# Kernel tuning notes

Hardware: AMD Instinct MI355X
Metric: run time of the kernel (lower is better)

The kernel has to match this reference:

```python
import jax, jax.numpy as jnp
import numpy as np

D_MODEL = 1024
N_HEADS = 2
D_FF = 4096
SEQ = 4096
HEAD_DIM = D_MODEL // N_HEADS
SCALE = HEAD_DIM ** 0.5
LN_EPS = 1e-5


def _layer_norm(x, g, b):
    mu = jnp.mean(x, axis=-1, keepdims=True)
    var = jnp.mean(jnp.square(x - mu), axis=-1, keepdims=True)
    return (x - mu) * jax.lax.rsqrt(var + LN_EPS) * g + b


def _gelu_tanh(x):
    # torch nn.GELU(approximate='tanh')
    c = np.sqrt(2.0 / np.pi).astype(np.float32)
    return 0.5 * x * (1.0 + jnp.tanh(c * (x + 0.044715 * x * x * x)))


def setup_inputs() -> dict:
    key = jax.random.key(0)
    ks = jax.random.split(key, 12)
    s = 1.0 / np.sqrt(D_MODEL)
    sf = 1.0 / np.sqrt(D_FF)
    inp = {
        "x": jax.random.normal(ks[0], (SEQ, D_MODEL), jnp.float32),
        "ln1_g": jnp.ones((D_MODEL,), jnp.float32),
        "ln1_b": jnp.zeros((D_MODEL,), jnp.float32),
        "wq": jax.random.normal(ks[1], (D_MODEL, D_MODEL), jnp.float32) * s,
        "bq": jnp.zeros((D_MODEL,), jnp.float32),
        "wk": jax.random.normal(ks[2], (D_MODEL, D_MODEL), jnp.float32) * s,
        "bk": jnp.zeros((D_MODEL,), jnp.float32),
        "wv": jax.random.normal(ks[3], (D_MODEL, D_MODEL), jnp.float32) * s,
        "bv": jnp.zeros((D_MODEL,), jnp.float32),
        "wo": jax.random.normal(ks[4], (D_MODEL, D_MODEL), jnp.float32) * s,
        "bo": jnp.zeros((D_MODEL,), jnp.float32),
        "ln2_g": jnp.ones((D_MODEL,), jnp.float32),
        "ln2_b": jnp.zeros((D_MODEL,), jnp.float32),
        "w1": jax.random.normal(ks[5], (D_FF, D_MODEL), jnp.float32) * s,
        "b1": jnp.zeros((D_FF,), jnp.float32),
        "w2": jax.random.normal(ks[6], (D_MODEL, D_FF), jnp.float32) * sf,
        "b2": jnp.zeros((D_MODEL,), jnp.float32),
    }
    return inp


def reference(x, ln1_g, ln1_b, wq, bq, wk, bk, wv, bv, wo, bo,
              ln2_g, ln2_b, w1, b1, w2, b2):
    S = x.shape[0]
    h = _layer_norm(x, ln1_g, ln1_b)
    # torch Linear: y = h @ W.T + b
    q = h @ wq.T + bq
    k = h @ wk.T + bk
    v = h @ wv.T + bv
    # chunk(2, dim=-1) == reshape last dim to (heads, head_dim)
    qh = q.reshape(S, N_HEADS, HEAD_DIM)
    kh = k.reshape(S, N_HEADS, HEAD_DIM)
    vh = v.reshape(S, N_HEADS, HEAD_DIM)
    scores = jnp.einsum('shd,thd->hst', qh, kh) / SCALE  # [H,S,S]
    attn = jax.nn.softmax(scores, axis=-1)
    o = jnp.einsum('hst,thd->shd', attn, vh).reshape(S, D_MODEL)
    x = x + (o @ wo.T + bo)
    h2 = _layer_norm(x, ln2_g, ln2_b)
    ff = _gelu_tanh(h2 @ w1.T + b1) @ w2.T + b2
    return x + ff
```

## Files before the change

### kernel.cpp

```cpp
#include <hip/hip_runtime.h>
#include <math.h>

#define SEQ 4096
#define DM  1024
#define DFF 4096
#define NH  2
#define HD  512

typedef unsigned short ushort_t;
typedef short  s16x8 __attribute__((ext_vector_type(8)));
typedef float  f32x4 __attribute__((ext_vector_type(4)));
typedef unsigned short u16x8 __attribute__((ext_vector_type(8)));

__device__ __forceinline__ float bf2f(unsigned short u) {
    return __uint_as_float(((unsigned)u) << 16);
}
__device__ __forceinline__ unsigned short f2bf(float f) {
    unsigned u = __float_as_uint(f);
    unsigned r = (u + 0x7fffu + ((u >> 16) & 1u)) >> 16;
    return (unsigned short)r;
}

__device__ __forceinline__ void async_load16(void* lds, const void* g) {
    __builtin_amdgcn_global_load_lds(
        (const __attribute__((address_space(1))) void*)g,
        (__attribute__((address_space(3))) void*)lds, 16, 0, 0);
}

template<bool HAS_BIAS, bool DO_GELU, bool HAS_RES, bool OUT_BF16, int SPLITS, int MODE>
__global__ __launch_bounds__(256)
void gemm_nt(const ushort_t* __restrict__ A, int lda,
             const ushort_t* __restrict__ B, int ldb,
             void* __restrict__ Cv, int ldc,
             const float* __restrict__ bias,
             const float* __restrict__ res, int ldres,
             int K, float alpha,
             size_t strA, size_t strB, size_t strC, size_t strBias,
             float* __restrict__ rowsum)
{
    __shared__ alignas(16) ushort_t sA[128 * 64];
    __shared__ alignas(16) ushort_t sB[128 * 64];

    const int z  = blockIdx.z;
    const int zb = z / SPLITS;
    const int ks = (z % SPLITS) * K;
    A += (size_t)zb * strA;
    B += (size_t)zb * strB;
    if (HAS_BIAS) bias += (size_t)zb * strBias;

    const int tid   = threadIdx.x;
    const int lane  = tid & 63;
    const int wave  = tid >> 6;
    const int waveM = wave >> 1, waveN = wave & 1;
    const int m0 = blockIdx.y * 128, n0 = blockIdx.x * 128;
    const int lr = lane & 15, quad = lane >> 4;

    f32x4 acc[4][4] = {};

    const ushort_t* Ag = A + (size_t)m0 * lda + ks;
    const ushort_t* Bg = B + (size_t)n0 * ldb + ks;

    const int ldRow = (lane >> 3);
    const int ldCol = (((lane & 7) ^ (lane >> 3)) * 8);

    for (int k0 = 0; k0 < K; k0 += 64) {
#pragma unroll
        for (int i = 0; i < 4; ++i) {
            int r = wave * 32 + i * 8 + ldRow;
            async_load16(&sA[(wave * 32 + i * 8) * 64],
                         Ag + (size_t)r * lda + k0 + ldCol);
            async_load16(&sB[(wave * 32 + i * 8) * 64],
                         Bg + (size_t)r * ldb + k0 + ldCol);
        }
        __syncthreads();

#pragma unroll
        for (int kk = 0; kk < 64; kk += 32) {
            const int pg = ((((kk >> 3) + quad) ^ (lr & 7)) << 3);
            s16x8 af[4], bfr[4];
#pragma unroll
            for (int mi = 0; mi < 4; ++mi)
                af[mi] = *(const s16x8*)&sA[(waveM * 64 + mi * 16 + lr) * 64 + pg];
#pragma unroll
            for (int ni = 0; ni < 4; ++ni)
                bfr[ni] = *(const s16x8*)&sB[(waveN * 64 + ni * 16 + lr) * 64 + pg];
#pragma unroll
            for (int mi = 0; mi < 4; ++mi)
#pragma unroll
                for (int ni = 0; ni < 4; ++ni)
                    acc[mi][ni] = __builtin_amdgcn_mfma_f32_16x16x32_bf16(
                        af[mi], bfr[ni], acc[mi][ni], 0, 0, 0);
        }
        __syncthreads();
    }

    float rs_part[4][4];
    if (MODE == 1) {
#pragma unroll
        for (int mi = 0; mi < 4; ++mi)
#pragma unroll
            for (int r = 0; r < 4; ++r) rs_part[mi][r] = 0.0f;
    }

#pragma unroll
    for (int mi = 0; mi < 4; ++mi) {
#pragma unroll
        for (int r = 0; r < 4; ++r) {
            int row = m0 + waveM * 64 + mi * 16 + quad * 4 + r;
#pragma unroll
            for (int ni = 0; ni < 4; ++ni) {
                int col = n0 + waveN * 64 + ni * 16 + lr;
                float v = acc[mi][ni][r] * alpha;
                if (HAS_BIAS) v += bias[col];
                if (DO_GELU) {
                    float xx = v;
                    float inner = 0.7978845608028654f * (xx + 0.044715f * xx * xx * xx);
                    v = 0.5f * xx * (1.0f + tanhf(inner));
                }
                if (HAS_RES) v += res[(size_t)row * ldres + col];
                if (OUT_BF16) {
                    ushort_t bs = f2bf(MODE == 1 ? __expf(v) : v);
                    if (MODE == 1) rs_part[mi][r] += bf2f(bs);
                    ((ushort_t*)Cv)[(size_t)z * strC + (size_t)row * ldc + col] = bs;
                } else {
                    ((float*)Cv)[(size_t)z * strC + (size_t)row * ldc + col] = v;
                }
            }
        }
    }

    if (MODE == 1) {
#pragma unroll
        for (int mi = 0; mi < 4; ++mi) {
#pragma unroll
            for (int r = 0; r < 4; ++r) {
                float s = rs_part[mi][r];
                s += __shfl_xor(s, 1);
                s += __shfl_xor(s, 2);
                s += __shfl_xor(s, 4);
                s += __shfl_xor(s, 8);
                if (lr == 0) {
                    int row = m0 + waveM * 64 + mi * 16 + quad * 4 + r;
                    atomicAdd(&rowsum[(size_t)zb * SEQ + row], s);
                }
            }
        }
    }
}

template<int S, bool HAS_BIAS, bool HAS_RES, bool OUT_BF16, bool DIV_RS>
__global__ __launch_bounds__(256)
void reduce_splitk(const float* __restrict__ P, size_t slab,
                   void* __restrict__ outv, int N, int ldout, int colStride,
                   const float* __restrict__ bias,
                   const float* __restrict__ res, int ldres,
                   const float* __restrict__ rowsum)
{
    const int z = blockIdx.z;
    const float* Pz = P + (size_t)z * S * slab;
    size_t i = ((size_t)blockIdx.x * 256 + threadIdx.x) * 4;
    if (i >= slab) return;
    int row = (int)(i / (size_t)N);
    int col = (int)(i - (size_t)row * N);
    float4 a = *(const float4*)(Pz + i);
#pragma unroll
    for (int s = 1; s < S; ++s) {
        float4 b = *(const float4*)(Pz + (size_t)s * slab + i);
        a.x += b.x; a.y += b.y; a.z += b.z; a.w += b.w;
    }
    if (DIV_RS) {
        float inv = 1.0f / rowsum[(size_t)z * SEQ + row];
        a.x *= inv; a.y *= inv; a.z *= inv; a.w *= inv;
    }
    int oc = z * colStride + col;
    if (HAS_BIAS) {
        a.x += bias[oc]; a.y += bias[oc + 1]; a.z += bias[oc + 2]; a.w += bias[oc + 3];
    }
    if (HAS_RES) {
        float4 r4 = *(const float4*)(res + (size_t)row * ldres + oc);
        a.x += r4.x; a.y += r4.y; a.z += r4.z; a.w += r4.w;
    }
    if (OUT_BF16) {
        ushort_t* o = (ushort_t*)outv + (size_t)row * ldout + oc;
        o[0] = f2bf(a.x); o[1] = f2bf(a.y); o[2] = f2bf(a.z); o[3] = f2bf(a.w);
    } else {
        *(float4*)((float*)outv + (size_t)row * ldout + oc) = a;
    }
}

__global__ __launch_bounds__(256)
void layernorm_kernel(const float* __restrict__ x, const float* __restrict__ g,
                      const float* __restrict__ b, ushort_t* __restrict__ out)
{
    int row = blockIdx.x;
    int tid = threadIdx.x;
    float4 v = ((const float4*)(x + (size_t)row * DM))[tid];
    float s1 = v.x + v.y + v.z + v.w;
    float s2 = v.x * v.x + v.y * v.y + v.z * v.z + v.w * v.w;
#pragma unroll
    for (int o = 32; o > 0; o >>= 1) {
        s1 += __shfl_down(s1, o);
        s2 += __shfl_down(s2, o);
    }
    __shared__ float r1[4], r2[4];
    if ((tid & 63) == 0) { r1[tid >> 6] = s1; r2[tid >> 6] = s2; }
    __syncthreads();
    s1 = r1[0] + r1[1] + r1[2] + r1[3];
    s2 = r2[0] + r2[1] + r2[2] + r2[3];
    float mu  = s1 * (1.0f / DM);
    float var = s2 * (1.0f / DM) - mu * mu;
    float rs  = rsqrtf(var + 1e-5f);
    float4 gg = ((const float4*)g)[tid];
    float4 bb = ((const float4*)b)[tid];
    ushort_t* o = out + (size_t)row * DM + tid * 4;
    o[0] = f2bf((v.x - mu) * rs * gg.x + bb.x);
    o[1] = f2bf((v.y - mu) * rs * gg.y + bb.y);
    o[2] = f2bf((v.z - mu) * rs * gg.z + bb.z);
    o[3] = f2bf((v.w - mu) * rs * gg.w + bb.w);
}

__global__ __launch_bounds__(256)
void prep_kernel(const float* __restrict__ wq, const float* __restrict__ wk,
                 const float* __restrict__ wv, const float* __restrict__ wo,
                 const float* __restrict__ w1, const float* __restrict__ w2,
                 ushort_t* __restrict__ WQ, ushort_t* __restrict__ WK,
                 ushort_t* __restrict__ WV, ushort_t* __restrict__ WO,
                 ushort_t* __restrict__ W1d, ushort_t* __restrict__ W2d,
                 const float* __restrict__ bq, const float* __restrict__ bk,
                 const float* __restrict__ bv, float* __restrict__ BQKV,
                 float* __restrict__ RSUM)
{
    const long S1   = (long)DM * DM / 4;
    const long SW   = 4 * S1;
    const long SBIG = (long)DFF * DM / 4;
    long i = (long)blockIdx.x * 256 + threadIdx.x;

    const float* src; ushort_t* dst; long off;
    if (i < SW) {
        long seg = i / S1; off = i - seg * S1;
        src = seg == 0 ? wq : seg == 1 ? wk : seg == 2 ? wv : wo;
        dst = seg == 0 ? WQ : seg == 1 ? WK : seg == 2 ? WV : WO;
    } else if (i < SW + SBIG) {
        off = i - SW; src = w1; dst = W1d;
    } else if (i < SW + 2 * SBIG) {
        off = i - SW - SBIG; src = w2; dst = W2d;
    } else {
        long j = i - (SW + 2 * SBIG);
        if (j < 3 * DM / 4) {
            long e = j * 4;
#pragma unroll
            for (int t = 0; t < 4; ++t) {
                long k = e + t;
                float v = k < DM ? bq[k] : k < 2 * DM ? bk[k - DM] : bv[k - 2 * DM];
                BQKV[k] = v;
            }
        } else if (j < 3 * DM / 4 + NH * SEQ / 4) {
            long k = (j - 3 * DM / 4) * 4;
            *(float4*)&RSUM[k] = make_float4(0.f, 0.f, 0.f, 0.f);
        }
        return;
    }
    float4 f = *(const float4*)(src + off * 4);
    ushort_t* d = dst + off * 4;
    d[0] = f2bf(f.x); d[1] = f2bf(f.y); d[2] = f2bf(f.z); d[3] = f2bf(f.w);
}

__global__ __launch_bounds__(256)
void transpose_head(const ushort_t* __restrict__ V, ushort_t* __restrict__ Vt)
{
    __shared__ ushort_t tile[64][65];
    int t0 = blockIdx.x * 64, d0 = blockIdx.y * 64, h = blockIdx.z;
    int tid = threadIdx.x;
    for (int i = tid; i < 64 * 64; i += 256) {
        int r = i >> 6, c = i & 63;
        tile[r][c] = V[(size_t)(t0 + r) * DM + h * HD + d0 + c];
    }
    __syncthreads();
    for (int i = tid; i < 64 * 64; i += 256) {
        int r = i >> 6, c = i & 63;
        Vt[(size_t)h * HD * SEQ + (size_t)(d0 + r) * SEQ + t0 + c] = tile[c][r];
    }
}

extern "C" void kernel_launch(void* const* d_in, const int* in_sizes, int n_in,
                              void* d_out, int out_size, void* d_ws, size_t ws_size,
                              hipStream_t stream)
{
    const float* x   = (const float*)d_in[0];
    const float* g1  = (const float*)d_in[1];
    const float* be1 = (const float*)d_in[2];
    const float* wq  = (const float*)d_in[3];
    const float* bq  = (const float*)d_in[4];
    const float* wk  = (const float*)d_in[5];
    const float* bk  = (const float*)d_in[6];
    const float* wv  = (const float*)d_in[7];
    const float* bv  = (const float*)d_in[8];
    const float* wo  = (const float*)d_in[9];
    const float* bo  = (const float*)d_in[10];
    const float* g2  = (const float*)d_in[11];
    const float* be2 = (const float*)d_in[12];
    const float* w1  = (const float*)d_in[13];
    const float* b1  = (const float*)d_in[14];
    const float* w2  = (const float*)d_in[15];
    const float* b2  = (const float*)d_in[16];
    float* out = (float*)d_out;

    char* ws = (char*)d_ws;
    const size_t MB = 1ull << 20;
    ushort_t* WQ   = (ushort_t*)(ws + 0 * MB);
    ushort_t* WK   = (ushort_t*)(ws + 2 * MB);
    ushort_t* WV   = (ushort_t*)(ws + 4 * MB);
    ushort_t* WO   = (ushort_t*)(ws + 6 * MB);
    ushort_t* W1   = (ushort_t*)(ws + 8 * MB);
    ushort_t* W2   = (ushort_t*)(ws + 16 * MB);
    ushort_t* H    = (ushort_t*)(ws + 24 * MB);
    ushort_t* Q    = (ushort_t*)(ws + 32 * MB);
    ushort_t* Kb   = (ushort_t*)(ws + 40 * MB);
    ushort_t* V    = (ushort_t*)(ws + 48 * MB);
    ushort_t* Vt   = (ushort_t*)(ws + 56 * MB);
    ushort_t* SC   = (ushort_t*)(ws + 64 * MB);
    ushort_t* O    = (ushort_t*)(ws + 128 * MB);
    float*    X1   = (float*)(ws + 136 * MB);
    float*    P    = (float*)(ws + 152 * MB);
    float*    BQKV = (float*)(ws + 216 * MB);
    float*    RSUM = (float*)(ws + 216 * MB + 16 * 1024);

    dim3 blk(256);

    {
        long total = 4L * DM * DM + 2L * DFF * DM;
        long n4 = total / 4 + 3 * DM / 4 + NH * SEQ / 4;
        prep_kernel<<<dim3((unsigned)((n4 + 255) / 256)), blk, 0, stream>>>(
            wq, wk, wv, wo, w1, w2, WQ, WK, WV, WO, W1, W2,
            bq, bk, bv, BQKV, RSUM);
    }

    layernorm_kernel<<<SEQ, 256, 0, stream>>>(x, g1, be1, H);

    gemm_nt<true, false, false, true, 1, 0><<<dim3(DM / 128, SEQ / 128, 3), blk, 0, stream>>>(
        H, DM, WQ, DM, Q, DM, BQKV, nullptr, 0, DM, 1.0f,
        0, (size_t)DM * DM, (size_t)SEQ * DM, (size_t)DM, nullptr);

    transpose_head<<<dim3(SEQ / 64, HD / 64, NH), blk, 0, stream>>>(V, Vt);

    const float scale = 0.044194173824159216f;
    gemm_nt<false, false, false, true, 1, 1><<<dim3(SEQ / 128, SEQ / 128, NH), blk, 0, stream>>>(
        Q, DM, Kb, DM, SC, SEQ, nullptr, nullptr, 0, HD, scale,
        (size_t)HD, (size_t)HD, (size_t)SEQ * SEQ, 0, RSUM);

    gemm_nt<false, false, false, false, 2, 0><<<dim3(HD / 128, SEQ / 128, NH * 2), blk, 0, stream>>>(
        SC, SEQ, Vt, SEQ, P, HD, nullptr, nullptr, 0, SEQ / 2, 1.0f,
        (size_t)SEQ * SEQ, (size_t)HD * SEQ, (size_t)SEQ * HD, 0, nullptr);
    reduce_splitk<2, false, false, true, true><<<dim3((SEQ * HD / 4) / 256, 1, NH), blk, 0, stream>>>(
        P, (size_t)SEQ * HD, O, HD, DM, HD, nullptr, nullptr, 0, RSUM);

    gemm_nt<false, false, false, false, 2, 0><<<dim3(DM / 128, SEQ / 128, 2), blk, 0, stream>>>(
        O, DM, WO, DM, P, DM, nullptr, nullptr, 0, DM / 2, 1.0f,
        0, 0, (size_t)SEQ * DM, 0, nullptr);
    reduce_splitk<2, true, true, false, false><<<dim3((SEQ * DM / 4) / 256, 1, 1), blk, 0, stream>>>(
        P, (size_t)SEQ * DM, X1, DM, DM, 0, bo, x, DM, nullptr);

    layernorm_kernel<<<SEQ, 256, 0, stream>>>(X1, g2, be2, H);

    ushort_t* F1 = SC;
    gemm_nt<true, true, false, true, 1, 0><<<dim3(DFF / 128, SEQ / 128, 1), blk, 0, stream>>>(
        H, DM, W1, DM, F1, DFF, b1, nullptr, 0, DM, 1.0f, 0, 0, 0, 0, nullptr);

    gemm_nt<false, false, false, false, 4, 0><<<dim3(DM / 128, SEQ / 128, 4), blk, 0, stream>>>(
        F1, DFF, W2, DFF, P, DM, nullptr, nullptr, 0, DFF / 4, 1.0f,
        0, 0, (size_t)SEQ * DM, 0, nullptr);
    reduce_splitk<4, true, true, false, false><<<dim3((SEQ * DM / 4) / 256, 1, 1), blk, 0, stream>>>(
        P, (size_t)SEQ * DM, out, DM, DM, 0, b2, X1, DM, nullptr);
}
```

Baseline: 468.5 us.

## Fuse V transpose into QKV epilogue, fuse reduce+LN2, add 256-row tiles

The QKV GEMM epilogue now writes V directly in transposed per-head layout, which removes the separate transpose kernel. The O-projection split-K reduction is fused with the second layernorm into one kernel. A BM=256 tile with 512 threads is added and used for the scores GEMM and the FFN1 GEMM. GELU tanh is rewritten as an exp-based sigmoid form, and the FFN2 split-K count drops from 4 to 2. The goal is fewer launches and less memory traffic, at the cost of larger blocks and a changed GELU numeric form.

```diff
diff --git a/kernel.cpp b/kernel.cpp
--- a/kernel.cpp
+++ b/kernel.cpp
@@ -27,8 +27,9 @@
         (__attribute__((address_space(3))) void*)lds, 16, 0, 0);
 }
 
-template<bool HAS_BIAS, bool DO_GELU, bool HAS_RES, bool OUT_BF16, int SPLITS, int MODE>
-__global__ __launch_bounds__(256)
+template<bool HAS_BIAS, bool DO_GELU, bool HAS_RES, bool OUT_BF16, int SPLITS,
+         int MODE, int BM, bool TRV>
+__global__ __launch_bounds__(BM == 256 ? 512 : 256)
 void gemm_nt(const ushort_t* __restrict__ A, int lda,
              const ushort_t* __restrict__ B, int ldb,
              void* __restrict__ Cv, int ldc,
@@ -36,9 +37,9 @@
              const float* __restrict__ res, int ldres,
              int K, float alpha,
              size_t strA, size_t strB, size_t strC, size_t strBias,
-             float* __restrict__ rowsum)
-{
-    __shared__ alignas(16) ushort_t sA[128 * 64];
+             float* __restrict__ rowsum, ushort_t* __restrict__ vt)
+{
+    __shared__ alignas(16) ushort_t sA[BM * 64];
     __shared__ alignas(16) ushort_t sB[128 * 64];
 
     const int z  = blockIdx.z;
@@ -52,7 +53,7 @@
     const int lane  = tid & 63;
     const int wave  = tid >> 6;
     const int waveM = wave >> 1, waveN = wave & 1;
-    const int m0 = blockIdx.y * 128, n0 = blockIdx.x * 128;
+    const int m0 = blockIdx.y * BM, n0 = blockIdx.x * 128;
     const int lr = lane & 15, quad = lane >> 4;
 
     f32x4 acc[4][4] = {};
@@ -62,6 +63,8 @@
 
     const int ldRow = (lane >> 3);
     const int ldCol = (((lane & 7) ^ (lane >> 3)) * 8);
+    const int NB = (BM == 256) ? 2 : 4;
+    const int BW = (BM == 256) ? 16 : 32;
 
     for (int k0 = 0; k0 < K; k0 += 64) {
 #pragma unroll
@@ -69,7 +72,11 @@
             int r = wave * 32 + i * 8 + ldRow;
             async_load16(&sA[(wave * 32 + i * 8) * 64],
                          Ag + (size_t)r * lda + k0 + ldCol);
-            async_load16(&sB[(wave * 32 + i * 8) * 64],
+        }
+#pragma unroll
+        for (int i = 0; i < NB; ++i) {
+            int r = wave * BW + i * 8 + ldRow;
+            async_load16(&sB[(wave * BW + i * 8) * 64],
                          Bg + (size_t)r * ldb + k0 + ldCol);
         }
         __syncthreads();
@@ -92,6 +99,30 @@
                         af[mi], bfr[ni], acc[mi][ni], 0, 0, 0);
         }
         __syncthreads();
+    }
+
+    if (TRV && zb == 2) {
+#pragma unroll
+        for (int mi = 0; mi < 4; ++mi) {
+#pragma unroll
+            for (int ni = 0; ni < 4; ++ni) {
+                int t0 = m0 + waveM * 64 + mi * 16 + quad * 4;
+                int col = n0 + waveN * 64 + ni * 16 + lr;
+                unsigned b[4];
+#pragma unroll
+                for (int r = 0; r < 4; ++r) {
+                    float v = acc[mi][ni][r] * alpha;
+                    if (HAS_BIAS) v += bias[col];
+                    b[r] = f2bf(v);
+                }
+                uint2 pk;
+                pk.x = b[0] | (b[1] << 16);
+                pk.y = b[2] | (b[3] << 16);
+                int h = col >> 9, d = col & (HD - 1);
+                *(uint2*)(vt + (size_t)h * HD * SEQ + (size_t)d * SEQ + t0) = pk;
+            }
+        }
+        return;
     }
 
     float rs_part[4][4];
@@ -114,8 +145,9 @@
                 if (HAS_BIAS) v += bias[col];
                 if (DO_GELU) {
                     float xx = v;
-                    float inner = 0.7978845608028654f * (xx + 0.044715f * xx * xx * xx);
-                    v = 0.5f * xx * (1.0f + tanhf(inner));
+                    float y2 = 1.5957691216057308f * (xx + 0.044715f * xx * xx * xx);
+                    float t = __expf(y2);
+                    v = xx * t / (t + 1.0f);
                 }
                 if (HAS_RES) v += res[(size_t)row * ldres + col];
                 if (OUT_BF16) {
@@ -186,6 +218,51 @@
     } else {
         *(float4*)((float*)outv + (size_t)row * ldout + oc) = a;
     }
+}
+
+__global__ __launch_bounds__(256)
+void reduce_oproj_ln(const float* __restrict__ P,
+                     const float* __restrict__ bo, const float* __restrict__ x,
+                     float* __restrict__ X1,
+                     const float* __restrict__ g, const float* __restrict__ b,
+                     ushort_t* __restrict__ H)
+{
+    int row = blockIdx.x;
+    int tid = threadIdx.x;
+    size_t off = (size_t)row * DM + tid * 4;
+    float4 p0 = *(const float4*)(P + off);
+    float4 p1 = *(const float4*)(P + (size_t)SEQ * DM + off);
+    float4 bb = ((const float4*)bo)[tid];
+    float4 xr = *(const float4*)(x + off);
+    float4 v;
+    v.x = p0.x + p1.x + bb.x + xr.x;
+    v.y = p0.y + p1.y + bb.y + xr.y;
+    v.z = p0.z + p1.z + bb.z + xr.z;
+    v.w = p0.w + p1.w + bb.w + xr.w;
+    *(float4*)(X1 + off) = v;
+
+    float s1 = v.x + v.y + v.z + v.w;
+    float s2 = v.x * v.x + v.y * v.y + v.z * v.z + v.w * v.w;
+#pragma unroll
+    for (int o = 32; o > 0; o >>= 1) {
+        s1 += __shfl_down(s1, o);
+        s2 += __shfl_down(s2, o);
+    }
+    __shared__ float r1[4], r2[4];
+    if ((tid & 63) == 0) { r1[tid >> 6] = s1; r2[tid >> 6] = s2; }
+    __syncthreads();
+    s1 = r1[0] + r1[1] + r1[2] + r1[3];
+    s2 = r2[0] + r2[1] + r2[2] + r2[3];
+    float mu  = s1 * (1.0f / DM);
+    float var = s2 * (1.0f / DM) - mu * mu;
+    float rs  = rsqrtf(var + 1e-5f);
+    float4 gg = ((const float4*)g)[tid];
+    float4 be = ((const float4*)b)[tid];
+    ushort_t* o = H + off;
+    o[0] = f2bf((v.x - mu) * rs * gg.x + be.x);
+    o[1] = f2bf((v.y - mu) * rs * gg.y + be.y);
+    o[2] = f2bf((v.z - mu) * rs * gg.z + be.z);
+    o[3] = f2bf((v.w - mu) * rs * gg.w + be.w);
 }
 
 __global__ __launch_bounds__(256)
@@ -263,23 +340,6 @@
     float4 f = *(const float4*)(src + off * 4);
     ushort_t* d = dst + off * 4;
     d[0] = f2bf(f.x); d[1] = f2bf(f.y); d[2] = f2bf(f.z); d[3] = f2bf(f.w);
-}
-
-__global__ __launch_bounds__(256)
-void transpose_head(const ushort_t* __restrict__ V, ushort_t* __restrict__ Vt)
-{
-    __shared__ ushort_t tile[64][65];
-    int t0 = blockIdx.x * 64, d0 = blockIdx.y * 64, h = blockIdx.z;
-    int tid = threadIdx.x;
-    for (int i = tid; i < 64 * 64; i += 256) {
-        int r = i >> 6, c = i & 63;
-        tile[r][c] = V[(size_t)(t0 + r) * DM + h * HD + d0 + c];
-    }
-    __syncthreads();
-    for (int i = tid; i < 64 * 64; i += 256) {
-        int r = i >> 6, c = i & 63;
-        Vt[(size_t)h * HD * SEQ + (size_t)(d0 + r) * SEQ + t0 + c] = tile[c][r];
-    }
 }
 
 extern "C" void kernel_launch(void* const* d_in, const int* in_sizes, int n_in,
@@ -324,8 +384,9 @@
     float*    P    = (float*)(ws + 152 * MB);
     float*    BQKV = (float*)(ws + 216 * MB);
     float*    RSUM = (float*)(ws + 216 * MB + 16 * 1024);
-
-    dim3 blk(256);
+    (void)V;
+
+    dim3 blk(256), blk2(512);
 
     {
         long total = 4L * DM * DM + 2L * DFF * DM;
@@ -337,38 +398,42 @@
 
     layernorm_kernel<<<SEQ, 256, 0, stream>>>(x, g1, be1, H);
 
-    gemm_nt<true, false, false, true, 1, 0><<<dim3(DM / 128, SEQ / 128, 3), blk, 0, stream>>>(
+    gemm_nt<true, false, false, true, 1, 0, 128, true>
+        <<<dim3(DM / 128, SEQ / 128, 3), blk, 0, stream>>>(
         H, DM, WQ, DM, Q, DM, BQKV, nullptr, 0, DM, 1.0f,
-        0, (size_t)DM * DM, (size_t)SEQ * DM, (size_t)DM, nullptr);
-
-    transpose_head<<<dim3(SEQ / 64, HD / 64, NH), blk, 0, stream>>>(V, Vt);
+        0, (size_t)DM * DM, (size_t)SEQ * DM, (size_t)DM, nullptr, Vt);
 
     const float scale = 0.044194173824159216f;
-    gemm_nt<false, false, false, true, 1, 1><<<dim3(SEQ / 128, SEQ / 128, NH), blk, 0, stream>>>(
+    gemm_nt<false, false, false, true, 1, 1, 256, false>
+        <<<dim3(SEQ / 128, SEQ / 256, NH), blk2, 0, stream>>>(
         Q, DM, Kb, DM, SC, SEQ, nullptr, nullptr, 0, HD, scale,
-        (size_t)HD, (size_t)HD, (size_t)SEQ * SEQ, 0, RSUM);
-
-    gemm_nt<false, false, false, false, 2, 0><<<dim3(HD / 128, SEQ / 128, NH * 2), blk, 0, stream>>>(
+        (size_t)HD, (size_t)HD, (size_t)SEQ * SEQ, 0, RSUM, nullptr);
+
+    gemm_nt<false, false, false, false, 2, 0, 128, false>
+        <<<dim3(HD / 128, SEQ / 128, NH * 2), blk, 0, stream>>>(
         SC, SEQ, Vt, SEQ, P, HD, nullptr, nullptr, 0, SEQ / 2, 1.0f,
-        (size_t)SEQ * SEQ, (size_t)HD * SEQ, (size_t)SEQ * HD, 0, nullptr);
-    reduce_splitk<2, false, false, true, true><<<dim3((SEQ * HD / 4) / 256, 1, NH), blk, 0, stream>>>(
+        (size_t)SEQ * SEQ, (size_t)HD * SEQ, (size_t)SEQ * HD, 0, nullptr, nullptr);
+    reduce_splitk<2, false, false, true, true>
+        <<<dim3((SEQ * HD / 4) / 256, 1, NH), blk, 0, stream>>>(
         P, (size_t)SEQ * HD, O, HD, DM, HD, nullptr, nullptr, 0, RSUM);
 
-    gemm_nt<false, false, false, false, 2, 0><<<dim3(DM / 128, SEQ / 128, 2), blk, 0, stream>>>(
+    gemm_nt<false, false, false, false, 2, 0, 128, false>
+        <<<dim3(DM / 128, SEQ / 128, 2), blk, 0, stream>>>(
         O, DM, WO, DM, P, DM, nullptr, nullptr, 0, DM / 2, 1.0f,
-        0, 0, (size_t)SEQ * DM, 0, nullptr);
-    reduce_splitk<2, true, true, false, false><<<dim3((SEQ * DM / 4) / 256, 1, 1), blk, 0, stream>>>(
-        P, (size_t)SEQ * DM, X1, DM, DM, 0, bo, x, DM, nullptr);
-
-    layernorm_kernel<<<SEQ, 256, 0, stream>>>(X1, g2, be2, H);
+        0, 0, (size_t)SEQ * DM, 0, nullptr, nullptr);
+    reduce_oproj_ln<<<SEQ, 256, 0, stream>>>(P, bo, x, X1, g2, be2, H);
 
     ushort_t* F1 = SC;
-    gemm_nt<true, true, false, true, 1, 0><<<dim3(DFF / 128, SEQ / 128, 1), blk, 0, stream>>>(
-        H, DM, W1, DM, F1, DFF, b1, nullptr, 0, DM, 1.0f, 0, 0, 0, 0, nullptr);
-
-    gemm_nt<false, false, false, false, 4, 0><<<dim3(DM / 128, SEQ / 128, 4), blk, 0, stream>>>(
-        F1, DFF, W2, DFF, P, DM, nullptr, nullptr, 0, DFF / 4, 1.0f,
-        0, 0, (size_t)SEQ * DM, 0, nullptr);
-    reduce_splitk<4, true, true, false, false><<<dim3((SEQ * DM / 4) / 256, 1, 1), blk, 0, stream>>>(
+    gemm_nt<true, true, false, true, 1, 0, 256, false>
+        <<<dim3(DFF / 128, SEQ / 256, 1), blk2, 0, stream>>>(
+        H, DM, W1, DM, F1, DFF, b1, nullptr, 0, DM, 1.0f, 0, 0, 0, 0,
+        nullptr, nullptr);
+
+    gemm_nt<false, false, false, false, 2, 0, 128, false>
+        <<<dim3(DM / 128, SEQ / 128, 2), blk, 0, stream>>>(
+        F1, DFF, W2, DFF, P, DM, nullptr, nullptr, 0, DFF / 2, 1.0f,
+        0, 0, (size_t)SEQ * DM, 0, nullptr, nullptr);
+    reduce_splitk<2, true, true, false, false>
+        <<<dim3((SEQ * DM / 4) / 256, 1, 1), blk, 0, stream>>>(
         P, (size_t)SEQ * DM, out, DM, DM, 0, b2, X1, DM, nullptr);
 }
```

Result: faster. 415.1 us (-11.4%).
